# Performance work log

Hardware: AMD Instinct MI355X
Metric: run time of the kernel (lower is better)

Reference implementation:

```python
import jax, jax.numpy as jnp
import numpy as np

EPS = 1e-7        # keras backend epsilon used by KLDivergence clipping
DELTA = 1.0       # tf.losses.huber default delta
ACTIVE_W = 1.0
BLANK_W = 1.0
KL_W = 0.1


def _huber_mean_last(y_true, y_pred):
    # tf.losses.huber: elementwise huber (delta=1), mean over last axis
    err = jnp.abs(y_pred - y_true)
    quad = jnp.minimum(err, DELTA)
    lin = err - quad
    return jnp.mean(0.5 * quad * quad + DELTA * lin, axis=-1)


def setup_inputs() -> dict:
    key = jax.random.key(0)
    k1, k2, k3 = jax.random.split(key, 3)
    B, T, H, W, C = 16, 1024, 14, 14, 16
    cam_output = jax.random.uniform(k1, (B, T, H, W, C), dtype=jnp.float32)
    count = jax.random.normal(k2, (B, C), dtype=jnp.float32) * 10.0
    length = jax.random.randint(k3, (B,), 1, T).astype(jnp.int64)
    return {"cam_output": cam_output, "count": count, "length": length}


def reference(cam_output, count, length):
    B, T, H, W, C = cam_output.shape
    # time mask replaces per-example dynamic slice + zero pad
    mask = (jnp.arange(T)[None, :] < length[:, None]).astype(cam_output.dtype)  # [B,T]
    m = mask[:, :, None, None, None]                                           # [B,T,1,1,1]

    active = cam_output * m          # == padded active_pred
    blank = cam_output * (1.0 - m)   # == padded blank_pred

    active_sum = jnp.sum(active, axis=(1, 2, 3))  # [B,C]
    blank_sum = jnp.sum(blank, axis=(1, 2, 3))    # [B,C]

    active_huber = _huber_mean_last(count, active_sum) * ACTIVE_W            # [B]
    blank_huber = _huber_mean_last(jnp.zeros_like(blank_sum), blank_sum) * BLANK_W  # [B]

    # uniform dist: ones_like(active_pred) / shape(active_pred)[1] == 1/H, zero-padded past length
    y_true = jnp.clip(m * (1.0 / H), EPS, 1.0)   # [B,T,1,1,1] (broadcasts over H,W,C)
    y_pred = jnp.clip(active, EPS, 1.0)          # [B,T,H,W,C]
    kl_per = jnp.sum(y_true * jnp.log(y_true / y_pred), axis=-1)  # [B,T,H,W]
    kl_loss = jnp.mean(kl_per) * KL_W            # scalar (keras mean reduction)

    return active_huber + blank_huber + kl_loss  # [B]
```

## Files before the change

kernel.cpp:

```cpp
#include <hip/hip_runtime.h>

#define BB 16
#define TT 1024
#define HH 14
#define WW 14
#define CC 16

constexpr int FL4_PER_T     = HH * WW * CC / 4;
constexpr int FL4_PER_BATCH = TT * FL4_PER_T;
constexpr int CHUNKS_PER_B  = 64;
constexpr int FL4_PER_CHUNK = FL4_PER_BATCH / CHUNKS_PER_B;
constexpr int T_PER_CHUNK   = TT / CHUNKS_PER_B;
constexpr int THREADS       = 256;
constexpr int ITERS         = FL4_PER_CHUNK / THREADS;
constexpr int NBLOCKS       = BB * CHUNKS_PER_B;

constexpr int WS_BLK_OFF = NBLOCKS * CC;
constexpr int WS_KL_OFF  = 2 * NBLOCKS * CC;

#define EPSF      1e-7f
#define INV_H     (1.0f / 14.0f)
#define LN_INV_H  (-2.63905732962f)

__device__ __forceinline__ void active_body(const float4 x,
    float& a0, float& a1, float& a2, float& a3, float& kl)
{
    a0 += x.x; a1 += x.y; a2 += x.z; a3 += x.w;
    float l0 = __logf(fminf(fmaxf(x.x, EPSF), 1.0f));
    float l1 = __logf(fminf(fmaxf(x.y, EPSF), 1.0f));
    float l2 = __logf(fminf(fmaxf(x.z, EPSF), 1.0f));
    float l3 = __logf(fminf(fmaxf(x.w, EPSF), 1.0f));
    kl += 4.0f * LN_INV_H - (l0 + l1 + l2 + l3);
}

__global__ __launch_bounds__(THREADS)
void ttv_sums_kernel(const float* __restrict__ cam,
                     const int*   __restrict__ length,
                     float* __restrict__ part)
{
    const int bid   = (int)blockIdx.x;
    const int b     = bid >> 6;
    const int chunk = bid & 63;
    const int len   = length[b];
    const int rel   = len - chunk * T_PER_CHUNK;

    const float4* __restrict__ base =
        reinterpret_cast<const float4*>(cam) + (size_t)bid * FL4_PER_CHUNK;

    float a0 = 0.f, a1 = 0.f, a2 = 0.f, a3 = 0.f;
    float q0 = 0.f, q1 = 0.f, q2 = 0.f, q3 = 0.f;
    float kl = 0.f;

    int idx = (int)threadIdx.x;

    if (rel >= T_PER_CHUNK) {
        #pragma unroll 4
        for (int it = 0; it < ITERS; ++it, idx += THREADS) {
            float4 x = base[idx];
            active_body(x, a0, a1, a2, a3, kl);
        }
    } else if (rel <= 0) {
        #pragma unroll 4
        for (int it = 0; it < ITERS; ++it, idx += THREADS) {
            float4 x = base[idx];
            q0 += x.x; q1 += x.y; q2 += x.z; q3 += x.w;
        }
    } else {
        #pragma unroll 4
        for (int it = 0; it < ITERS; ++it, idx += THREADS) {
            float4 x = base[idx];
            int tl = idx / FL4_PER_T;
            if (tl < rel) {
                active_body(x, a0, a1, a2, a3, kl);
            } else {
                q0 += x.x; q1 += x.y; q2 += x.z; q3 += x.w;
            }
        }
    }

    #pragma unroll
    for (int off = 4; off <= 32; off <<= 1) {
        a0 += __shfl_xor(a0, off); a1 += __shfl_xor(a1, off);
        a2 += __shfl_xor(a2, off); a3 += __shfl_xor(a3, off);
        q0 += __shfl_xor(q0, off); q1 += __shfl_xor(q1, off);
        q2 += __shfl_xor(q2, off); q3 += __shfl_xor(q3, off);
    }
    #pragma unroll
    for (int off = 1; off <= 32; off <<= 1) kl += __shfl_xor(kl, off);

    __shared__ float s_red[2 * CC + 1];
    if (threadIdx.x < 2 * CC + 1) s_red[threadIdx.x] = 0.f;
    __syncthreads();

    const int lane = (int)(threadIdx.x & 63u);
    if (lane < 4) {
        const int cb = lane * 4;
        atomicAdd(&s_red[cb + 0], a0); atomicAdd(&s_red[cb + 1], a1);
        atomicAdd(&s_red[cb + 2], a2); atomicAdd(&s_red[cb + 3], a3);
        atomicAdd(&s_red[CC + cb + 0], q0); atomicAdd(&s_red[CC + cb + 1], q1);
        atomicAdd(&s_red[CC + cb + 2], q2); atomicAdd(&s_red[CC + cb + 3], q3);
    }
    if (lane == 0) atomicAdd(&s_red[2 * CC], kl * INV_H);
    __syncthreads();

    if (threadIdx.x < CC) {
        part[bid * CC + (int)threadIdx.x] = s_red[threadIdx.x];
    } else if (threadIdx.x < 2 * CC) {
        part[WS_BLK_OFF + bid * CC + (int)threadIdx.x - CC] = s_red[threadIdx.x];
    } else if (threadIdx.x == 2 * CC) {
        part[WS_KL_OFF + bid] = s_red[2 * CC];
    }
}

__global__ __launch_bounds__(THREADS)
void ttv_finalize_kernel(const float* __restrict__ part,
                         const float* __restrict__ count,
                         float* __restrict__ out)
{
    const int tid = (int)threadIdx.x;
    const int b = tid >> 4;
    const int c = tid & 15;

    float as = 0.f, bs = 0.f;
    #pragma unroll
    for (int k = 0; k < CHUNKS_PER_B; ++k) {
        const int row = (b * CHUNKS_PER_B + k) * CC + c;
        as += part[row];
        bs += part[WS_BLK_OFF + row];
    }

    float kl = 0.f;
    #pragma unroll
    for (int k = tid; k < NBLOCKS; k += THREADS) kl += part[WS_KL_OFF + k];
    #pragma unroll
    for (int off = 1; off <= 32; off <<= 1) kl += __shfl_xor(kl, off);
    __shared__ float s_kl[4];
    if ((tid & 63) == 0) s_kl[tid >> 6] = kl;
    __syncthreads();
    const float klsum = s_kl[0] + s_kl[1] + s_kl[2] + s_kl[3];

    const float cnt = count[tid];
    float ea = fabsf(as - cnt);
    float qa = fminf(ea, 1.0f);
    float ha = 0.5f * qa * qa + (ea - qa);
    float eb = fabsf(bs);
    float qb = fminf(eb, 1.0f);
    float hb = 0.5f * qb * qb + (eb - qb);

    float h = ha + hb;
    #pragma unroll
    for (int off = 1; off < 16; off <<= 1) h += __shfl_xor(h, off);

    if (c == 0) {
        const float kl_loss = klsum * (0.1f / (float)(BB * TT * HH * WW));
        out[b] = h * (1.0f / 16.0f) + kl_loss;
    }
}

extern "C" void kernel_launch(void* const* d_in, const int* in_sizes, int n_in,
                              void* d_out, int out_size, void* d_ws, size_t ws_size,
                              hipStream_t stream)
{
    const float* cam    = (const float*)d_in[0];
    const float* count  = (const float*)d_in[1];
    const int*   length = (const int*)d_in[2];
    float* out  = (float*)d_out;
    float* part = (float*)d_ws;

    ttv_sums_kernel<<<NBLOCKS, THREADS, 0, stream>>>(cam, length, part);
    ttv_finalize_kernel<<<1, THREADS, 0, stream>>>(part, count, out);
}
```

Before: 45.60 us.

## Fuse finalize into sums kernel via last-block atomic counter; combine logs via product

```diff
diff --git a/kernel.cpp b/kernel.cpp
--- a/kernel.cpp
+++ b/kernel.cpp
@@ -15,8 +15,9 @@
 constexpr int ITERS         = FL4_PER_CHUNK / THREADS;
 constexpr int NBLOCKS       = BB * CHUNKS_PER_B;
 
-constexpr int WS_BLK_OFF = NBLOCKS * CC;
-constexpr int WS_KL_OFF  = 2 * NBLOCKS * CC;
+constexpr int WS_BLK = NBLOCKS * CC;
+constexpr int WS_KL  = 2 * NBLOCKS * CC;
+constexpr int WS_CTR = WS_KL + NBLOCKS;
 
 #define EPSF      1e-7f
 #define INV_H     (1.0f / 14.0f)
@@ -26,17 +27,19 @@
     float& a0, float& a1, float& a2, float& a3, float& kl)
 {
     a0 += x.x; a1 += x.y; a2 += x.z; a3 += x.w;
-    float l0 = __logf(fminf(fmaxf(x.x, EPSF), 1.0f));
-    float l1 = __logf(fminf(fmaxf(x.y, EPSF), 1.0f));
-    float l2 = __logf(fminf(fmaxf(x.z, EPSF), 1.0f));
-    float l3 = __logf(fminf(fmaxf(x.w, EPSF), 1.0f));
-    kl += 4.0f * LN_INV_H - (l0 + l1 + l2 + l3);
+    float c0 = fminf(fmaxf(x.x, EPSF), 1.0f);
+    float c1 = fminf(fmaxf(x.y, EPSF), 1.0f);
+    float c2 = fminf(fmaxf(x.z, EPSF), 1.0f);
+    float c3 = fminf(fmaxf(x.w, EPSF), 1.0f);
+    kl += 4.0f * LN_INV_H - __logf((c0 * c1) * (c2 * c3));
 }
 
 __global__ __launch_bounds__(THREADS)
-void ttv_sums_kernel(const float* __restrict__ cam,
-                     const int*   __restrict__ length,
-                     float* __restrict__ part)
+void ttv_fused_kernel(const float* __restrict__ cam,
+                      const int*   __restrict__ length,
+                      const float* __restrict__ count,
+                      float* __restrict__ part,
+                      float* __restrict__ out)
 {
     const int bid   = (int)blockIdx.x;
     const int b     = bid >> 6;
@@ -104,40 +107,45 @@
     __syncthreads();
 
     if (threadIdx.x < CC) {
-        part[bid * CC + (int)threadIdx.x] = s_red[threadIdx.x];
+        part[chunk * 256 + b * CC + (int)threadIdx.x] = s_red[threadIdx.x];
     } else if (threadIdx.x < 2 * CC) {
-        part[WS_BLK_OFF + bid * CC + (int)threadIdx.x - CC] = s_red[threadIdx.x];
+        part[WS_BLK + chunk * 256 + b * CC + (int)threadIdx.x - CC] = s_red[threadIdx.x];
     } else if (threadIdx.x == 2 * CC) {
-        part[WS_KL_OFF + bid] = s_red[2 * CC];
+        part[WS_KL + bid] = s_red[2 * CC];
     }
-}
+    __syncthreads();
 
-__global__ __launch_bounds__(THREADS)
-void ttv_finalize_kernel(const float* __restrict__ part,
-                         const float* __restrict__ count,
-                         float* __restrict__ out)
-{
+    __shared__ int s_last;
+    if (threadIdx.x == 0) {
+        __threadfence();
+        unsigned int old = atomicAdd((unsigned int*)(part + WS_CTR), 1u);
+        s_last = (old == (unsigned int)(NBLOCKS - 1)) ? 1 : 0;
+    }
+    __syncthreads();
+    if (!s_last) return;
+
+    __threadfence();
+
     const int tid = (int)threadIdx.x;
-    const int b = tid >> 4;
-    const int c = tid & 15;
+    const int fb  = tid >> 4;
+    const int fc  = tid & 15;
 
     float as = 0.f, bs = 0.f;
     #pragma unroll
     for (int k = 0; k < CHUNKS_PER_B; ++k) {
-        const int row = (b * CHUNKS_PER_B + k) * CC + c;
-        as += part[row];
-        bs += part[WS_BLK_OFF + row];
+        as += part[k * 256 + tid];
+        bs += part[WS_BLK + k * 256 + tid];
     }
 
-    float kl = 0.f;
+    float klp = 0.f;
     #pragma unroll
-    for (int k = tid; k < NBLOCKS; k += THREADS) kl += part[WS_KL_OFF + k];
+    for (int j = 0; j < 4; ++j) klp += part[WS_KL + j * 256 + tid];
     #pragma unroll
-    for (int off = 1; off <= 32; off <<= 1) kl += __shfl_xor(kl, off);
-    __shared__ float s_kl[4];
-    if ((tid & 63) == 0) s_kl[tid >> 6] = kl;
+    for (int off = 1; off <= 32; off <<= 1) klp += __shfl_xor(klp, off);
+    __shared__ float s_klw[4];
+    if ((tid & 63) == 0) s_klw[tid >> 6] = klp;
     __syncthreads();
-    const float klsum = s_kl[0] + s_kl[1] + s_kl[2] + s_kl[3];
+    const float klsum = s_klw[0] + s_klw[1] + s_klw[2] + s_klw[3];
 
     const float cnt = count[tid];
     float ea = fabsf(as - cnt);
@@ -149,11 +157,11 @@
 
     float h = ha + hb;
     #pragma unroll
-    for (int off = 1; off < 16; off <<= 1) h += __shfl_xor(h, off);
+    for (int off = 1; off <= 8; off <<= 1) h += __shfl_xor(h, off);
 
-    if (c == 0) {
+    if (fc == 0) {
         const float kl_loss = klsum * (0.1f / (float)(BB * TT * HH * WW));
-        out[b] = h * (1.0f / 16.0f) + kl_loss;
+        out[fb] = h * (1.0f / 16.0f) + kl_loss;
     }
 }
 
@@ -167,6 +175,7 @@
     float* out  = (float*)d_out;
     float* part = (float*)d_ws;
 
-    ttv_sums_kernel<<<NBLOCKS, THREADS, 0, stream>>>(cam, length, part);
-    ttv_finalize_kernel<<<1, THREADS, 0, stream>>>(part, count, out);
+    hipMemsetAsync((char*)d_ws + (size_t)WS_CTR * sizeof(float), 0, 4, stream);
+
+    ttv_fused_kernel<<<NBLOCKS, THREADS, 0, stream>>>(cam, length, count, part, out);
 }
```

Result: slower. 79.27 us (+73.8%).
